# Kernel tuning notes

Hardware: AMD Instinct MI355X
Metric: run time of the kernel (lower is better)

## Reference

```python
import jax, jax.numpy as jnp
import numpy as np

N, K, D = 8192, 64, 256          # nodes, edges per dst node, feat_dim
RATE = 0.5                        # denoise_topK_rate
SET0 = int(K * (1.0 - RATE))      # edges dropped per row (lowest keep-prob)


def setup_inputs() -> dict:
    key = jax.random.key(0)
    ks = jax.random.split(key, 6)
    # K unique, sorted neighbors per row (sorted => pair ordering matches
    # torch's row-major nonzero() on a dense adjacency)
    nbr = jax.vmap(lambda k: jax.random.permutation(k, N)[:K])(
        jax.random.split(ks[0], N))
    nbr = jnp.sort(nbr, axis=1).astype(jnp.int32)
    vals = jax.random.uniform(ks[1], (N, K), minval=0.1, maxval=1.0)
    adj = jnp.zeros((N, N), jnp.float32).at[jnp.arange(N)[:, None], nbr].set(vals)
    feat = jax.random.normal(ks[2], (N, D), dtype=jnp.float32)
    # keep_cls params: Linear(D, D//2) -> PReLU(D//2) -> Linear(D//2, 2)
    W1 = jax.random.normal(ks[3], (D, D // 2), dtype=jnp.float32) / np.float32(np.sqrt(D))
    b1 = jnp.zeros((D // 2,), jnp.float32)
    prelu_a = jnp.full((D // 2,), 0.25, jnp.float32)  # torch PReLU default init
    W2 = jax.random.normal(ks[4], (D // 2, 2), dtype=jnp.float32) / np.float32(np.sqrt(D // 2))
    b2 = jnp.zeros((2,), jnp.float32)
    return {"adj": adj, "feat": feat, "nbr_idx": nbr, "dst_num": N,
            "W1": W1, "b1": b1, "prelu_a": prelu_a, "W2": W2, "b2": b2}


def reference(adj, feat, nbr_idx, dst_num, W1, b1, prelu_a, W2, b2):
    dst = dst_num  # == adj.shape[0]; every dst row has exactly K nonzeros
    rows = jnp.arange(dst, dtype=jnp.int32)[:, None]            # [dst,1]
    pair_src = jnp.repeat(jnp.arange(dst, dtype=jnp.int32), K)  # [E]
    pair_dst = nbr_idx.reshape(-1)                              # [E]
    pair_list = jnp.stack([pair_src, pair_dst], axis=1)         # [E,2]
    before_edge_num = jnp.float32(pair_list.shape[0]) / dst

    # edge MLP on feature differences
    diff = feat[pair_src] - feat[pair_dst]                      # [E,D]
    h = diff @ W1 + b1
    h = jnp.where(h >= 0, h, prelu_a * h)                       # PReLU
    prob_arr = jax.nn.softmax(h @ W2 + b2, axis=1)              # [E,2]

    # segmented (per-dst-row) argsort of keep-prob; drop SET0 lowest
    p1 = prob_arr[:, 1].reshape(dst, K)                         # [dst,K]
    order = jnp.argsort(p1, axis=1)                             # ascending
    drop_cols = jnp.take_along_axis(nbr_idx, order[:, :SET0], axis=1)
    adj2 = adj.at[rows, drop_cols].set(0.0)
    left_row = (rows * K + order[:, SET0:]).reshape(-1)         # kept edge ids
    after_edge_num = jnp.count_nonzero(adj2).astype(jnp.float32) / dst

    # degree-normalize
    degrees = jnp.sum(adj2, axis=1)
    new_adj = adj2 / (degrees[:, None] + 1e-6)
    return (new_adj, feat, prob_arr, pair_list, before_edge_num,
            after_edge_num, left_row)
```

## Files before the change

### kernel.cpp

```cpp
#include <hip/hip_runtime.h>
#include <cmath>

#define NN 8192
#define KK 64
#define DD 256
#define HH 128
#define SET0V 32
#define EE (NN*KK)

static constexpr size_t OFF_ADJ  = 0;
static constexpr size_t OFF_FEAT = (size_t)NN * NN;
static constexpr size_t OFF_PROB = OFF_FEAT + (size_t)NN * DD;
static constexpr size_t OFF_PAIR = OFF_PROB + (size_t)EE * 2;
static constexpr size_t OFF_BEF  = OFF_PAIR + (size_t)EE * 2;
static constexpr size_t OFF_AFT  = OFF_BEF + 1;
static constexpr size_t OFF_LEFT = OFF_AFT + 1;

__global__ __launch_bounds__(128) void k_g(const float* __restrict__ feat,
                                           const float* __restrict__ W1,
                                           double* __restrict__ g,
                                           float4* __restrict__ out_feat,
                                           float* __restrict__ out_scal) {
  __shared__ float sf[8 * DD];
  int j = threadIdx.x;
  int n0 = blockIdx.x * 8;
  const float4* fsrc = (const float4*)(feat + (size_t)n0 * DD);
  float4* fdst = (float4*)sf;
  float4* odst = out_feat + (size_t)n0 * DD / 4;
#pragma unroll
  for (int t = 0; t < 4; t++) {
    float4 v = fsrc[j + t * 128];
    fdst[j + t * 128] = v;
    odst[j + t * 128] = v;
  }
  if (blockIdx.x == 0 && j == 0) {
    out_scal[0] = 64.0f;
    out_scal[1] = 32.0f;
  }
  __syncthreads();
  double acc[8];
#pragma unroll
  for (int n = 0; n < 8; n++) acc[n] = 0.0;
  for (int k = 0; k < DD; k += 4) {
    double w0 = (double)W1[(k + 0) * HH + j];
    double w1 = (double)W1[(k + 1) * HH + j];
    double w2 = (double)W1[(k + 2) * HH + j];
    double w3 = (double)W1[(k + 3) * HH + j];
#pragma unroll
    for (int n = 0; n < 8; n++) {
      float4 f = *(const float4*)&sf[n * DD + k];
      acc[n] += (double)f.x * w0;
      acc[n] += (double)f.y * w1;
      acc[n] += (double)f.z * w2;
      acc[n] += (double)f.w * w3;
    }
  }
#pragma unroll
  for (int n = 0; n < 8; n++) g[(size_t)(n0 + n) * HH + j] = acc[n];
}

__global__ __launch_bounds__(256) void k_edge(
    const double* __restrict__ g, const int* __restrict__ nbr,
    const float* __restrict__ b1, const float* __restrict__ b2,
    const float* __restrict__ pa, const float* __restrict__ W2,
    double* __restrict__ p1d, float* __restrict__ out_prob,
    float* __restrict__ out_pair) {
  int wave = threadIdx.x >> 6;
  int lane = threadIdx.x & 63;
  int r = blockIdx.x * 4 + wave;
  int q = lane >> 4;
  int s = lane & 15;

  double grb[8], aa[8], w0c[8], w1c[8];
  const double* gr = g + (size_t)r * HH + s * 8;
#pragma unroll
  for (int d = 0; d < 8; d++) {
    int dim = s * 8 + d;
    grb[d] = gr[d] + (double)b1[dim];
    aa[d]  = (double)pa[dim];
    w0c[d] = (double)W2[2 * dim];
    w1c[d] = (double)W2[2 * dim + 1];
  }

  const int* nrow = nbr + r * KK;
  double st0 = 0.0, st1 = 0.0;
  for (int grp = 0; grp < 16; grp++) {
    int c = nrow[grp * 4 + q];
    const double* gc = g + (size_t)c * HH + s * 8;
    double t0 = 0.0, t1 = 0.0;
#pragma unroll
    for (int d = 0; d < 8; d++) {
      double h = grb[d] - gc[d];
      h = h >= 0.0 ? h : aa[d] * h;
      t0 += h * w0c[d];
      t1 += h * w1c[d];
    }
#pragma unroll
    for (int m = 1; m < 16; m <<= 1) {
      t0 += __shfl_xor(t0, m, 16);
      t1 += __shfl_xor(t1, m, 16);
    }
    if (s == grp) { st0 = t0; st1 = t1; }
  }
  int src = ((lane & 3) << 4) | (lane >> 2);
  double T0 = __shfl(st0, src, 64);
  double T1 = __shfl(st1, src, 64);
  double l0 = T0 + (double)b2[0];
  double l1 = T1 + (double)b2[1];
  double m = l0 > l1 ? l0 : l1;
  double e0 = exp(l0 - m), e1 = exp(l1 - m);
  double inv = 1.0 / (e0 + e1);
  size_t e = (size_t)r * KK + lane;
  int c = nrow[lane];
  p1d[e] = e1 * inv;
  *(float2*)(out_prob + 2 * e) = make_float2((float)(e0 * inv), (float)(e1 * inv));
  *(float2*)(out_pair + 2 * e) = make_float2((float)r, (float)c);
}

__global__ __launch_bounds__(256) void k_adj(
    const double* __restrict__ p1d, const int* __restrict__ nbr,
    const float* __restrict__ adj, float* __restrict__ out_adj,
    float* __restrict__ out_left) {
  int r = blockIdx.x;
  int t = threadIdx.x;
  float4* row4 = (float4*)(out_adj + (size_t)r * NN);
  float4 z = make_float4(0.f, 0.f, 0.f, 0.f);
#pragma unroll
  for (int i = 0; i < 8; i++) row4[t + i * 256] = z;

  __shared__ double sp[KK];
  __shared__ double sm[KK];
  double p = 0.0;
  float v = 0.f;
  int c = 0;
  if (t < KK) {
    p = p1d[(size_t)r * KK + t];
    sp[t] = p;
    c = nbr[r * KK + t];
    v = adj[(size_t)r * NN + c];
  }
  __syncthreads();
  int rank = 0;
  if (t < KK) {
#pragma unroll 8
    for (int j = 0; j < KK; j++) {
      double qq = sp[j];
      rank += (int)((qq < p) || (qq == p && j < t));
    }
    sm[t] = (rank >= SET0V) ? (double)v : 0.0;
  }
  __syncthreads();
  if (t < KK) {
    double deg = 0.0;
#pragma unroll 8
    for (int j = 0; j < KK; j++) deg += sm[j];
    if (rank >= SET0V) {
      out_adj[(size_t)r * NN + c] = (float)((double)v / (deg + 1e-6));
      out_left[(size_t)r * SET0V + (rank - SET0V)] = (float)(r * KK + t);
    }
  }
}

extern "C" void kernel_launch(void* const* d_in, const int* in_sizes, int n_in,
                              void* d_out, int out_size, void* d_ws, size_t ws_size,
                              hipStream_t stream) {
  const float* adj  = (const float*)d_in[0];
  const float* feat = (const float*)d_in[1];
  const int*   nbr  = (const int*)d_in[2];
  const float* W1   = (const float*)d_in[4];
  const float* b1   = (const float*)d_in[5];
  const float* pa   = (const float*)d_in[6];
  const float* W2   = (const float*)d_in[7];
  const float* b2   = (const float*)d_in[8];
  float* out = (float*)d_out;

  double* g   = (double*)d_ws;
  double* p1d = g + (size_t)NN * HH;

  hipLaunchKernelGGL(k_g, dim3(1024), dim3(128), 0, stream,
                     feat, W1, g, (float4*)(out + OFF_FEAT), out + OFF_BEF);
  hipLaunchKernelGGL(k_edge, dim3(2048), dim3(256), 0, stream,
                     g, nbr, b1, b2, pa, W2,
                     p1d, out + OFF_PROB, out + OFF_PAIR);
  hipLaunchKernelGGL(k_adj, dim3(8192), dim3(256), 0, stream,
                     p1d, nbr, adj, out + OFF_ADJ, out + OFF_LEFT);
}
```

Baseline: 528.7 us.

## Zero adjacency rows inside edge kernel with nontemporal stores, compact rank kernel

The 256MB zero-fill of the output adjacency moves from the rank kernel into the edge-MLP kernel, where it is interleaved with the compute loop and uses nontemporal stores. The goal is to overlap the bandwidth-bound fill with edge math. The rank kernel now handles four rows per block, one per wave, and ranks on the logit difference instead of the softmax probability. Softmax is computed in float, and the feature copy and adjacency gather also use nontemporal accesses. Ranking on l1-l0 in double keeps the sort order, but the float softmax outputs may differ slightly from the old double path.

New measurement: 513.2 us. 2.9% less time.

```diff
diff --git a/kernel.cpp b/kernel.cpp
--- a/kernel.cpp
+++ b/kernel.cpp
@@ -7,6 +7,8 @@
 #define HH 128
 #define SET0V 32
 #define EE (NN*KK)
+
+typedef float f4_t __attribute__((ext_vector_type(4)));
 
 static constexpr size_t OFF_ADJ  = 0;
 static constexpr size_t OFF_FEAT = (size_t)NN * NN;
@@ -19,19 +21,19 @@
 __global__ __launch_bounds__(128) void k_g(const float* __restrict__ feat,
                                            const float* __restrict__ W1,
                                            double* __restrict__ g,
-                                           float4* __restrict__ out_feat,
+                                           f4_t* __restrict__ out_feat,
                                            float* __restrict__ out_scal) {
   __shared__ float sf[8 * DD];
   int j = threadIdx.x;
   int n0 = blockIdx.x * 8;
-  const float4* fsrc = (const float4*)(feat + (size_t)n0 * DD);
-  float4* fdst = (float4*)sf;
-  float4* odst = out_feat + (size_t)n0 * DD / 4;
+  const f4_t* fsrc = (const f4_t*)(feat + (size_t)n0 * DD);
+  f4_t* fdst = (f4_t*)sf;
+  f4_t* odst = out_feat + (size_t)n0 * DD / 4;
 #pragma unroll
   for (int t = 0; t < 4; t++) {
-    float4 v = fsrc[j + t * 128];
+    f4_t v = fsrc[j + t * 128];
     fdst[j + t * 128] = v;
-    odst[j + t * 128] = v;
+    __builtin_nontemporal_store(v, odst + j + t * 128);
   }
   if (blockIdx.x == 0 && j == 0) {
     out_scal[0] = 64.0f;
@@ -48,7 +50,7 @@
     double w3 = (double)W1[(k + 3) * HH + j];
 #pragma unroll
     for (int n = 0; n < 8; n++) {
-      float4 f = *(const float4*)&sf[n * DD + k];
+      f4_t f = *(const f4_t*)&sf[n * DD + k];
       acc[n] += (double)f.x * w0;
       acc[n] += (double)f.y * w1;
       acc[n] += (double)f.z * w2;
@@ -64,12 +66,15 @@
     const float* __restrict__ b1, const float* __restrict__ b2,
     const float* __restrict__ pa, const float* __restrict__ W2,
     double* __restrict__ p1d, float* __restrict__ out_prob,
-    float* __restrict__ out_pair) {
+    float* __restrict__ out_pair, float* __restrict__ out_adj) {
   int wave = threadIdx.x >> 6;
   int lane = threadIdx.x & 63;
   int r = blockIdx.x * 4 + wave;
   int q = lane >> 4;
   int s = lane & 15;
+
+  f4_t* row4 = (f4_t*)(out_adj + (size_t)r * NN);
+  const f4_t z = {0.f, 0.f, 0.f, 0.f};
 
   double grb[8], aa[8], w0c[8], w1c[8];
   const double* gr = g + (size_t)r * HH + s * 8;
@@ -85,6 +90,9 @@
   const int* nrow = nbr + r * KK;
   double st0 = 0.0, st1 = 0.0;
   for (int grp = 0; grp < 16; grp++) {
+    __builtin_nontemporal_store(z, row4 + lane + (2 * grp) * 64);
+    __builtin_nontemporal_store(z, row4 + lane + (2 * grp + 1) * 64);
+
     int c = nrow[grp * 4 + q];
     const double* gc = g + (size_t)c * HH + s * 8;
     double t0 = 0.0, t1 = 0.0;
@@ -107,57 +115,45 @@
   double T1 = __shfl(st1, src, 64);
   double l0 = T0 + (double)b2[0];
   double l1 = T1 + (double)b2[1];
-  double m = l0 > l1 ? l0 : l1;
-  double e0 = exp(l0 - m), e1 = exp(l1 - m);
-  double inv = 1.0 / (e0 + e1);
   size_t e = (size_t)r * KK + lane;
   int c = nrow[lane];
-  p1d[e] = e1 * inv;
-  *(float2*)(out_prob + 2 * e) = make_float2((float)(e0 * inv), (float)(e1 * inv));
+  p1d[e] = l1 - l0;
+  float dm = (float)(l0 > l1 ? l0 : l1);
+  float e0 = expf((float)l0 - dm), e1 = expf((float)l1 - dm);
+  float inv = 1.0f / (e0 + e1);
+  *(float2*)(out_prob + 2 * e) = make_float2(e0 * inv, e1 * inv);
   *(float2*)(out_pair + 2 * e) = make_float2((float)r, (float)c);
 }
 
-__global__ __launch_bounds__(256) void k_adj(
+__global__ __launch_bounds__(256) void k_rank(
     const double* __restrict__ p1d, const int* __restrict__ nbr,
     const float* __restrict__ adj, float* __restrict__ out_adj,
     float* __restrict__ out_left) {
-  int r = blockIdx.x;
-  int t = threadIdx.x;
-  float4* row4 = (float4*)(out_adj + (size_t)r * NN);
-  float4 z = make_float4(0.f, 0.f, 0.f, 0.f);
-#pragma unroll
-  for (int i = 0; i < 8; i++) row4[t + i * 256] = z;
-
-  __shared__ double sp[KK];
-  __shared__ double sm[KK];
-  double p = 0.0;
-  float v = 0.f;
-  int c = 0;
-  if (t < KK) {
-    p = p1d[(size_t)r * KK + t];
-    sp[t] = p;
-    c = nbr[r * KK + t];
-    v = adj[(size_t)r * NN + c];
-  }
+  int wave = threadIdx.x >> 6;
+  int lane = threadIdx.x & 63;
+  int r = blockIdx.x * 4 + wave;
+  __shared__ double sp[4][64];
+  __shared__ double sv[4][64];
+  double p = p1d[(size_t)r * KK + lane];
+  sp[wave][lane] = p;
+  int c = nbr[r * KK + lane];
+  float v = __builtin_nontemporal_load(&adj[(size_t)r * NN + c]);
   __syncthreads();
   int rank = 0;
-  if (t < KK) {
 #pragma unroll 8
-    for (int j = 0; j < KK; j++) {
-      double qq = sp[j];
-      rank += (int)((qq < p) || (qq == p && j < t));
-    }
-    sm[t] = (rank >= SET0V) ? (double)v : 0.0;
+  for (int j = 0; j < KK; j++) {
+    double qq = sp[wave][j];
+    rank += (int)((qq < p) || (qq == p && j < lane));
   }
+  bool kept = rank >= SET0V;
+  sv[wave][lane] = kept ? (double)v : 0.0;
   __syncthreads();
-  if (t < KK) {
-    double deg = 0.0;
+  double deg = 0.0;
 #pragma unroll 8
-    for (int j = 0; j < KK; j++) deg += sm[j];
-    if (rank >= SET0V) {
-      out_adj[(size_t)r * NN + c] = (float)((double)v / (deg + 1e-6));
-      out_left[(size_t)r * SET0V + (rank - SET0V)] = (float)(r * KK + t);
-    }
+  for (int j = 0; j < KK; j++) deg += sv[wave][j];
+  if (kept) {
+    out_adj[(size_t)r * NN + c] = (float)((double)v / (deg + 1e-6));
+    out_left[(size_t)r * SET0V + (rank - SET0V)] = (float)(r * KK + lane);
   }
 }
 
@@ -178,10 +174,10 @@
   double* p1d = g + (size_t)NN * HH;
 
   hipLaunchKernelGGL(k_g, dim3(1024), dim3(128), 0, stream,
-                     feat, W1, g, (float4*)(out + OFF_FEAT), out + OFF_BEF);
+                     feat, W1, g, (f4_t*)(out + OFF_FEAT), out + OFF_BEF);
   hipLaunchKernelGGL(k_edge, dim3(2048), dim3(256), 0, stream,
                      g, nbr, b1, b2, pa, W2,
-                     p1d, out + OFF_PROB, out + OFF_PAIR);
-  hipLaunchKernelGGL(k_adj, dim3(8192), dim3(256), 0, stream,
+                     p1d, out + OFF_PROB, out + OFF_PAIR, out + OFF_ADJ);
+  hipLaunchKernelGGL(k_rank, dim3(2048), dim3(256), 0, stream,
                      p1d, nbr, adj, out + OFF_ADJ, out + OFF_LEFT);
 }
```
